# Performance work log

Measured on AMD Instinct MI355X. Metric: run time of the kernel, lower is better.

Reference implementation:

```python
import jax, jax.numpy as jnp
import numpy as np

NODE_DIM = 512
PROMPT_DIM = 512
N_NODES = 100000
N_GRAPHS = 1024


def setup_inputs() -> dict:
    key = jax.random.key(0)
    k1, k2, k3, k4, k5, k6, k7 = jax.random.split(key, 7)
    node_feats = jax.random.normal(k1, (N_NODES, NODE_DIM), dtype=jnp.float32)
    graph_prompt = jax.random.normal(k2, (N_GRAPHS, PROMPT_DIM), dtype=jnp.float32)
    batch_idx = jnp.sort(jax.random.randint(k3, (N_NODES,), 0, N_GRAPHS))
    # Linear init ~ U(-1/sqrt(fan_in), 1/sqrt(fan_in)) like torch defaults
    fan1 = NODE_DIM + PROMPT_DIM
    b1 = 1.0 / np.sqrt(fan1)
    W1 = jax.random.uniform(k4, (fan1, NODE_DIM), minval=-b1, maxval=b1, dtype=jnp.float32)
    bias1 = jax.random.uniform(k5, (NODE_DIM,), minval=-b1, maxval=b1, dtype=jnp.float32)
    b2 = 1.0 / np.sqrt(NODE_DIM)
    W2 = jax.random.uniform(k6, (NODE_DIM, NODE_DIM), minval=-b2, maxval=b2, dtype=jnp.float32)
    bias2 = jax.random.uniform(k7, (NODE_DIM,), minval=-b2, maxval=b2, dtype=jnp.float32)
    return {"node_feats": node_feats, "graph_prompt": graph_prompt, "batch_idx": batch_idx,
            "W1": W1, "bias1": bias1, "W2": W2, "bias2": bias2}


def reference(node_feats, graph_prompt, batch_idx, W1, bias1, W2, bias2):
    # gather per-node prompt: [N, prompt_dim]
    prompt_expanded = graph_prompt[batch_idx]
    combined = jnp.concatenate([node_feats, prompt_expanded], axis=-1)  # [N, node_dim+prompt_dim]
    h = jax.nn.relu(combined @ W1 + bias1)  # [N, node_dim]
    return h @ W2 + bias2  # [N, node_dim]
```

## Files before the change

### kernel.cpp

```cpp
#include <hip/hip_runtime.h>


#define N_NODES 100000
#define MT1 782
#define NWG (MT1 * 4)

typedef __bf16 bf16x8 __attribute__((ext_vector_type(8)));
typedef float  f32x4  __attribute__((ext_vector_type(4)));
typedef unsigned short ushort_t;

__device__ __forceinline__ ushort_t f2bf(float f) {
  __bf16 b = (__bf16)f;
  return __builtin_bit_cast(unsigned short, b);
}

__device__ __forceinline__ bf16x8 cvt8(const float* p) {
  float4 x = *(const float4*)p;
  float4 y = *(const float4*)(p + 4);
  bf16x8 v;
  v[0] = (__bf16)x.x; v[1] = (__bf16)x.y; v[2] = (__bf16)x.z; v[3] = (__bf16)x.w;
  v[4] = (__bf16)y.x; v[5] = (__bf16)y.y; v[6] = (__bf16)y.z; v[7] = (__bf16)y.w;
  return v;
}

__device__ __forceinline__ void gload_lds16(const void* g, void* l) {
  __builtin_amdgcn_global_load_lds(
      (const __attribute__((address_space(1))) void*)g,
      (__attribute__((address_space(3))) void*)l, 16, 0, 0);
}

__global__ __launch_bounds__(256) void convert_kernel(const float* __restrict__ nf,
                                                      ushort_t* __restrict__ nfbf) {
  for (int c = blockIdx.x * 256 + threadIdx.x; c < 6400000; c += 2048 * 256)
    *(bf16x8*)(nfbf + (size_t)c * 8) = cvt8(nf + (size_t)c * 8);
}

__global__ void prep_kernel(const float* __restrict__ W1, const float* __restrict__ W2,
                            ushort_t* __restrict__ W1T, ushort_t* __restrict__ W2T) {
  int i = blockIdx.x * 256 + threadIdx.x;
  if (i < 524288) {
    int n = i >> 10, k = i & 1023;
    W1T[i] = f2bf(W1[k * 512 + n]);
  } else if (i < 786432) {
    int j = i - 524288;
    int n = j >> 9, k = j & 511;
    W2T[j] = f2bf(W2[k * 512 + n]);
  }
}

__global__ __launch_bounds__(256, 4) void p2_kernel(
    const float* __restrict__ gp, const ushort_t* __restrict__ W1T,
    const float* __restrict__ bias1, float* __restrict__ P2) {
  const int tid = threadIdx.x, lane = tid & 63, wid = tid >> 6;
  const int lc = lane & 15, lr = lane >> 4;
  const int m0 = (blockIdx.x >> 1) * 32;
  const int col0 = (blockIdx.x & 1) * 256 + wid * 64;

  f32x4 acc[2][4];
#pragma unroll
  for (int i = 0; i < 2; ++i)
#pragma unroll
    for (int j = 0; j < 4; ++j) acc[i][j] = {0.f, 0.f, 0.f, 0.f};

  const float* a0 = gp + (size_t)(m0 + lc) * 512;
  const ushort_t* bb = W1T + (size_t)(col0 + lc) * 1024 + 512;

#pragma unroll 2
  for (int kt = 0; kt < 8; ++kt) {
    bf16x8 bfr[2][4];
#pragma unroll
    for (int kk = 0; kk < 2; ++kk)
#pragma unroll
      for (int j = 0; j < 4; ++j)
        bfr[kk][j] = *(const bf16x8*)(bb + (size_t)j * 16 * 1024 + kt * 64 + kk * 32 + lr * 8);
    bf16x8 af[2][2];
#pragma unroll
    for (int i = 0; i < 2; ++i)
#pragma unroll
      for (int kk = 0; kk < 2; ++kk)
        af[i][kk] = cvt8(a0 + (size_t)i * 16 * 512 + kt * 64 + kk * 32 + lr * 8);
#pragma unroll
    for (int kk = 0; kk < 2; ++kk)
#pragma unroll
      for (int i = 0; i < 2; ++i)
#pragma unroll
        for (int j = 0; j < 4; ++j)
          acc[i][j] = __builtin_amdgcn_mfma_f32_16x16x32_bf16(af[i][kk], bfr[kk][j], acc[i][j], 0, 0, 0);
  }

#pragma unroll
  for (int i = 0; i < 2; ++i)
#pragma unroll
    for (int r = 0; r < 4; ++r) {
      int row = m0 + i * 16 + lr * 4 + r;
#pragma unroll
      for (int j = 0; j < 4; ++j) {
        int col = col0 + j * 16 + lc;
        P2[(size_t)row * 512 + col] = acc[i][j][r] + bias1[col];
      }
    }
}

__global__ __launch_bounds__(256, 2) void g1_kernel(
    const ushort_t* __restrict__ nfbf, const int* __restrict__ bidx,
    const ushort_t* __restrict__ W1T, const float* __restrict__ P2,
    ushort_t* __restrict__ h) {
  __shared__ ushort_t sA[128 * 64];
  __shared__ ushort_t sB[128 * 64];

  const int tid = threadIdx.x, lane = tid & 63, wid = tid >> 6;
  const int tile = (blockIdx.x & 7) * 391 + (blockIdx.x >> 3);
  const int m0 = (tile >> 2) * 128, n0 = (tile & 3) * 128;

  const ushort_t* pA[4]; const ushort_t* pB[4]; int ldsW[4];
#pragma unroll
  for (int s = 0; s < 4; ++s) {
    int q = wid * 256 + s * 64 + lane;
    int row = q >> 3;
    int cw = (q & 7) ^ (row & 7);
    int rowg = m0 + row; if (rowg > N_NODES - 1) rowg = N_NODES - 1;
    pA[s] = nfbf + (size_t)rowg * 512 + cw * 8;
    pB[s] = W1T + (size_t)(n0 + row) * 1024 + cw * 8;
    ldsW[s] = (wid * 256 + s * 64) * 8;
  }

  f32x4 acc[4][4];
#pragma unroll
  for (int i = 0; i < 4; ++i)
#pragma unroll
    for (int j = 0; j < 4; ++j) acc[i][j] = {0.f, 0.f, 0.f, 0.f};

  const int wm = (wid >> 1) * 64, wn = (wid & 1) * 64;
  const int lr = lane >> 4, lc = lane & 15;

  for (int kt = 0; kt < 8; ++kt) {
#pragma unroll
    for (int s = 0; s < 4; ++s) {
      gload_lds16(pA[s], &sA[ldsW[s]]); pA[s] += 64;
      gload_lds16(pB[s], &sB[ldsW[s]]); pB[s] += 64;
    }
    __syncthreads();
#pragma unroll
    for (int kk = 0; kk < 2; ++kk) {
      bf16x8 af[4], bfr[4];
#pragma unroll
      for (int i = 0; i < 4; ++i) {
        int row = wm + i * 16 + lc;
        int cp = (kk * 4 + lr) ^ (row & 7);
        af[i] = *(const bf16x8*)&sA[row * 64 + cp * 8];
      }
#pragma unroll
      for (int j = 0; j < 4; ++j) {
        int col = wn + j * 16 + lc;
        int cp = (kk * 4 + lr) ^ (col & 7);
        bfr[j] = *(const bf16x8*)&sB[col * 64 + cp * 8];
      }
#pragma unroll
      for (int i = 0; i < 4; ++i)
#pragma unroll
        for (int j = 0; j < 4; ++j)
          acc[i][j] = __builtin_amdgcn_mfma_f32_16x16x32_bf16(af[i], bfr[j], acc[i][j], 0, 0, 0);
    }
    __syncthreads();
  }

#pragma unroll
  for (int i = 0; i < 4; ++i) {
#pragma unroll
    for (int r = 0; r < 4; ++r) {
      int row = m0 + wm + i * 16 + lr * 4 + r;
      if (row < N_NODES) {
        int g = bidx[row];
        const float* p2r = P2 + (size_t)g * 512 + n0 + wn;
#pragma unroll
        for (int j = 0; j < 4; ++j) {
          float v = fmaxf(acc[i][j][r] + p2r[j * 16 + lc], 0.f);
          h[(size_t)row * 512 + n0 + wn + j * 16 + lc] = f2bf(v);
        }
      }
    }
  }
}

__global__ __launch_bounds__(256, 2) void g2_kernel(
    const ushort_t* __restrict__ h, const ushort_t* __restrict__ W2T,
    const float* __restrict__ bias2, float* __restrict__ out) {
  __shared__ ushort_t sA[128 * 64];
  __shared__ ushort_t sB[128 * 64];

  const int tid = threadIdx.x, lane = tid & 63, wid = tid >> 6;
  const int tile = (blockIdx.x & 7) * 391 + (blockIdx.x >> 3);
  const int m0 = (tile >> 2) * 128, n0 = (tile & 3) * 128;

  const ushort_t* pA[4]; const ushort_t* pB[4]; int ldsW[4];
#pragma unroll
  for (int s = 0; s < 4; ++s) {
    int q = wid * 256 + s * 64 + lane;
    int row = q >> 3;
    int cw = (q & 7) ^ (row & 7);
    int rowg = m0 + row; if (rowg > N_NODES - 1) rowg = N_NODES - 1;
    pA[s] = h + (size_t)rowg * 512 + cw * 8;
    pB[s] = W2T + (size_t)(n0 + row) * 512 + cw * 8;
    ldsW[s] = (wid * 256 + s * 64) * 8;
  }

  f32x4 acc[4][4];
#pragma unroll
  for (int i = 0; i < 4; ++i)
#pragma unroll
    for (int j = 0; j < 4; ++j) acc[i][j] = {0.f, 0.f, 0.f, 0.f};

  const int wm = (wid >> 1) * 64, wn = (wid & 1) * 64;
  const int lr = lane >> 4, lc = lane & 15;

  for (int kt = 0; kt < 8; ++kt) {
#pragma unroll
    for (int s = 0; s < 4; ++s) {
      gload_lds16(pA[s], &sA[ldsW[s]]); pA[s] += 64;
      gload_lds16(pB[s], &sB[ldsW[s]]); pB[s] += 64;
    }
    __syncthreads();
#pragma unroll
    for (int kk = 0; kk < 2; ++kk) {
      bf16x8 af[4], bfr[4];
#pragma unroll
      for (int i = 0; i < 4; ++i) {
        int row = wm + i * 16 + lc;
        int cp = (kk * 4 + lr) ^ (row & 7);
        af[i] = *(const bf16x8*)&sA[row * 64 + cp * 8];
      }
#pragma unroll
      for (int j = 0; j < 4; ++j) {
        int col = wn + j * 16 + lc;
        int cp = (kk * 4 + lr) ^ (col & 7);
        bfr[j] = *(const bf16x8*)&sB[col * 64 + cp * 8];
      }
#pragma unroll
      for (int i = 0; i < 4; ++i)
#pragma unroll
        for (int j = 0; j < 4; ++j)
          acc[i][j] = __builtin_amdgcn_mfma_f32_16x16x32_bf16(af[i], bfr[j], acc[i][j], 0, 0, 0);
    }
    __syncthreads();
  }

#pragma unroll
  for (int j = 0; j < 4; ++j) {
    int col = n0 + wn + j * 16 + lc;
    float bv = bias2[col];
#pragma unroll
    for (int i = 0; i < 4; ++i)
#pragma unroll
      for (int r = 0; r < 4; ++r) {
        int row = m0 + wm + i * 16 + lr * 4 + r;
        if (row < N_NODES) out[(size_t)row * 512 + col] = acc[i][j][r] + bv;
      }
  }
}

extern "C" void kernel_launch(void* const* d_in, const int* in_sizes, int n_in,
                              void* d_out, int out_size, void* d_ws, size_t ws_size,
                              hipStream_t stream) {
  const float* nf   = (const float*)d_in[0];
  const float* gp   = (const float*)d_in[1];
  const int*   bidx = (const int*)d_in[2];
  const float* W1   = (const float*)d_in[3];
  const float* b1   = (const float*)d_in[4];
  const float* W2   = (const float*)d_in[5];
  const float* b2   = (const float*)d_in[6];
  float* out = (float*)d_out;

  char* ws = (char*)d_ws;
  ushort_t* W1T = (ushort_t*)ws;
  ushort_t* W2T = (ushort_t*)(ws + 1048576);
  float*    P2  = (float*)   (ws + 1572864);
  ushort_t* hbf = (ushort_t*)(ws + 3670016);

  ushort_t* nfbf = (ushort_t*)d_out;

  convert_kernel<<<2048, 256, 0, stream>>>(nf, nfbf);
  prep_kernel<<<3072, 256, 0, stream>>>(W1, W2, W1T, W2T);
  p2_kernel<<<64, 256, 0, stream>>>(gp, W1T, b1, P2);
  g1_kernel<<<NWG, 256, 0, stream>>>(nfbf, bidx, W1T, P2, hbf);
  g2_kernel<<<NWG, 256, 0, stream>>>(hbf, W2T, b2, out);
}
```

Baseline: 297.7 us.

## Fuse fp32-to-bf16 node feature conversion into first GEMM's LDS load path

Drops the separate conversion kernel that wrote a bf16 copy of node_feats. The first GEMM now loads fp32 rows straight into LDS with a 16-way XOR swizzle and converts to bf16 when reading fragments. This removes a full read and write pass over the 200MB input, at the cost of doubling the A-tile LDS footprint and global traffic inside g1. Each n-tile re-reads A as fp32, so g1 reads more bytes. Launch-bound occupancy hints also rise, to 3 for g1 and 4 for g2.

```diff
diff --git a/kernel.cpp b/kernel.cpp
--- a/kernel.cpp
+++ b/kernel.cpp
@@ -23,16 +23,17 @@
   return v;
 }
 
+__device__ __forceinline__ bf16x8 cvt8v(float4 x, float4 y) {
+  bf16x8 v;
+  v[0] = (__bf16)x.x; v[1] = (__bf16)x.y; v[2] = (__bf16)x.z; v[3] = (__bf16)x.w;
+  v[4] = (__bf16)y.x; v[5] = (__bf16)y.y; v[6] = (__bf16)y.z; v[7] = (__bf16)y.w;
+  return v;
+}
+
 __device__ __forceinline__ void gload_lds16(const void* g, void* l) {
   __builtin_amdgcn_global_load_lds(
       (const __attribute__((address_space(1))) void*)g,
       (__attribute__((address_space(3))) void*)l, 16, 0, 0);
-}
-
-__global__ __launch_bounds__(256) void convert_kernel(const float* __restrict__ nf,
-                                                      ushort_t* __restrict__ nfbf) {
-  for (int c = blockIdx.x * 256 + threadIdx.x; c < 6400000; c += 2048 * 256)
-    *(bf16x8*)(nfbf + (size_t)c * 8) = cvt8(nf + (size_t)c * 8);
 }
 
 __global__ void prep_kernel(const float* __restrict__ W1, const float* __restrict__ W2,
@@ -101,27 +102,35 @@
     }
 }
 
-__global__ __launch_bounds__(256, 2) void g1_kernel(
-    const ushort_t* __restrict__ nfbf, const int* __restrict__ bidx,
+__global__ __launch_bounds__(256, 3) void g1_kernel(
+    const float* __restrict__ nf, const int* __restrict__ bidx,
     const ushort_t* __restrict__ W1T, const float* __restrict__ P2,
     ushort_t* __restrict__ h) {
-  __shared__ ushort_t sA[128 * 64];
+  __shared__ float    sAf[128 * 64];
   __shared__ ushort_t sB[128 * 64];
 
   const int tid = threadIdx.x, lane = tid & 63, wid = tid >> 6;
   const int tile = (blockIdx.x & 7) * 391 + (blockIdx.x >> 3);
   const int m0 = (tile >> 2) * 128, n0 = (tile & 3) * 128;
 
-  const ushort_t* pA[4]; const ushort_t* pB[4]; int ldsW[4];
+  const float* pA[8]; int ldsA[8];
+#pragma unroll
+  for (int s = 0; s < 8; ++s) {
+    int q = s * 256 + tid;
+    int row = q >> 4;
+    int cw = (q & 15) ^ (row & 15);
+    int rowg = m0 + row; if (rowg > N_NODES - 1) rowg = N_NODES - 1;
+    pA[s] = nf + (size_t)rowg * 512 + cw * 4;
+    ldsA[s] = (s * 256 + wid * 64) * 4;
+  }
+  const ushort_t* pB[4]; int ldsB[4];
 #pragma unroll
   for (int s = 0; s < 4; ++s) {
     int q = wid * 256 + s * 64 + lane;
     int row = q >> 3;
     int cw = (q & 7) ^ (row & 7);
-    int rowg = m0 + row; if (rowg > N_NODES - 1) rowg = N_NODES - 1;
-    pA[s] = nfbf + (size_t)rowg * 512 + cw * 8;
     pB[s] = W1T + (size_t)(n0 + row) * 1024 + cw * 8;
-    ldsW[s] = (wid * 256 + s * 64) * 8;
+    ldsB[s] = (wid * 256 + s * 64) * 8;
   }
 
   f32x4 acc[4][4];
@@ -135,19 +144,23 @@
 
   for (int kt = 0; kt < 8; ++kt) {
 #pragma unroll
-    for (int s = 0; s < 4; ++s) {
-      gload_lds16(pA[s], &sA[ldsW[s]]); pA[s] += 64;
-      gload_lds16(pB[s], &sB[ldsW[s]]); pB[s] += 64;
-    }
-    __syncthreads();
+    for (int s = 0; s < 8; ++s) { gload_lds16(pA[s], &sAf[ldsA[s]]); pA[s] += 64; }
+#pragma unroll
+    for (int s = 0; s < 4; ++s) { gload_lds16(pB[s], &sB[ldsB[s]]); pB[s] += 64; }
+    __syncthreads();
+
 #pragma unroll
     for (int kk = 0; kk < 2; ++kk) {
       bf16x8 af[4], bfr[4];
 #pragma unroll
       for (int i = 0; i < 4; ++i) {
         int row = wm + i * 16 + lc;
-        int cp = (kk * 4 + lr) ^ (row & 7);
-        af[i] = *(const bf16x8*)&sA[row * 64 + cp * 8];
+        int c0 = kk * 8 + lr * 2;
+        int p0 = c0 ^ (row & 15);
+        int p1 = (c0 + 1) ^ (row & 15);
+        float4 x = *(const float4*)&sAf[row * 64 + p0 * 4];
+        float4 y = *(const float4*)&sAf[row * 64 + p1 * 4];
+        af[i] = cvt8v(x, y);
       }
 #pragma unroll
       for (int j = 0; j < 4; ++j) {
@@ -182,7 +195,7 @@
   }
 }
 
-__global__ __launch_bounds__(256, 2) void g2_kernel(
+__global__ __launch_bounds__(256, 4) void g2_kernel(
     const ushort_t* __restrict__ h, const ushort_t* __restrict__ W2T,
     const float* __restrict__ bias2, float* __restrict__ out) {
   __shared__ ushort_t sA[128 * 64];
@@ -276,11 +289,8 @@
   float*    P2  = (float*)   (ws + 1572864);
   ushort_t* hbf = (ushort_t*)(ws + 3670016);
 
-  ushort_t* nfbf = (ushort_t*)d_out;
-
-  convert_kernel<<<2048, 256, 0, stream>>>(nf, nfbf);
   prep_kernel<<<3072, 256, 0, stream>>>(W1, W2, W1T, W2T);
   p2_kernel<<<64, 256, 0, stream>>>(gp, W1T, b1, P2);
-  g1_kernel<<<NWG, 256, 0, stream>>>(nfbf, bidx, W1T, P2, hbf);
+  g1_kernel<<<NWG, 256, 0, stream>>>(nf, bidx, W1T, P2, hbf);
   g2_kernel<<<NWG, 256, 0, stream>>>(hbf, W2T, b2, out);
 }
```

Measured after the change: 295.2 us. About the same (-0.8%).
